# Kernel tuning notes

Hardware: AMD Instinct MI355X
Metric: run time of the kernel (lower is better)

## Reference

```python
import jax, jax.numpy as jnp
import numpy as np

EPS = 1e-6
H = 12  # num_heads


def _rms(x, w):
    return x / jnp.sqrt(jnp.mean(x * x, axis=-1, keepdims=True) + EPS) * w


def _rot_half(x):
    x1, x2 = jnp.split(x, 2, axis=-1)
    return jnp.concatenate([-x2, x1], axis=-1)


def _rope(t, cos, sin):
    # t: [B,H,N,hd]; cos/sin: [N,hd] broadcast
    return t * cos + _rot_half(t) * sin


def setup_inputs() -> dict:
    key = jax.random.key(0)
    B, N, D, Nc = 1, 2048, 768, 16
    hd = D // H
    mh = 4 * D
    ks = jax.random.split(key, 16)
    s = 0.02
    g = lambda k, shape, sc=1.0: jax.random.normal(k, shape, dtype=jnp.float32) * sc
    # real RoPE tables (half-duplicated layout to match rotate_half)
    inv = 1.0 / (10000.0 ** (np.arange(hd // 2, dtype=np.float64) / (hd // 2)))
    ang = np.arange(N, dtype=np.float64)[:, None] * inv[None, :]
    cos = jnp.asarray(np.concatenate([np.cos(ang), np.cos(ang)], -1), dtype=jnp.float32)
    sin = jnp.asarray(np.concatenate([np.sin(ang), np.sin(ang)], -1), dtype=jnp.float32)
    return {
        'x': g(ks[0], (B, N, D)),
        'c': g(ks[1], (B, D)),
        'cond': g(ks[2], (B, Nc, D)),
        'rope_cos': cos,
        'rope_sin': sin,
        'norm1_w': jnp.ones((D,), jnp.float32),
        'norm2_w': jnp.ones((D,), jnp.float32),
        'norm3_w': jnp.ones((D,), jnp.float32),
        'cond_norm_w': jnp.ones((D,), jnp.float32),
        'sa_qkv_w': g(ks[3], (3 * D, D), s),
        'sa_proj_w': g(ks[4], (D, D), s),
        'sa_proj_b': jnp.zeros((D,), jnp.float32),
        'sa_qn_w': jnp.ones((hd,), jnp.float32),
        'sa_kn_w': jnp.ones((hd,), jnp.float32),
        'ca_q_w': g(ks[5], (D, D), s),
        'ca_k_w': g(ks[6], (D, D), s),
        'ca_v_w': g(ks[7], (D, D), s),
        'ca_proj_w': g(ks[8], (D, D), s),
        'ca_proj_b': jnp.zeros((D,), jnp.float32),
        'ca_qn_w': jnp.ones((hd,), jnp.float32),
        'ca_kn_w': jnp.ones((hd,), jnp.float32),
        'mlp_w1': g(ks[9], (mh, D), s),
        'mlp_w2': g(ks[10], (D, mh), s),
        'mlp_w3': g(ks[11], (mh, D), s),
        'ada_w': g(ks[12], (9 * D, D), s),
        'ada_b': jnp.zeros((9 * D,), jnp.float32),
    }


def reference(x, c, cond, rope_cos, rope_sin, norm1_w, norm2_w, norm3_w, cond_norm_w,
              sa_qkv_w, sa_proj_w, sa_proj_b, sa_qn_w, sa_kn_w,
              ca_q_w, ca_k_w, ca_v_w, ca_proj_w, ca_proj_b, ca_qn_w, ca_kn_w,
              mlp_w1, mlp_w2, mlp_w3, ada_w, ada_b):
    B, N, D = x.shape
    hd = D // H
    scale = hd ** -0.5

    # adaLN modulation: SiLU(c) -> Linear -> 9 chunks of [B, D]
    mod = jax.nn.silu(c) @ ada_w.T + ada_b
    (sh_msa, sc_msa, g_msa, sh_ca, sc_ca, g_ca,
     sh_mlp, sc_mlp, g_mlp) = jnp.split(mod, 9, axis=1)

    def modulate(h, sh, sc):
        return h * (1.0 + sc[:, None, :]) + sh[:, None, :]

    # ---- self-attention with QK-norm + RoPE ----
    h = modulate(_rms(x, norm1_w), sh_msa, sc_msa)
    qkv = (h @ sa_qkv_w.T).reshape(B, N, 3, H, hd).transpose(2, 0, 3, 1, 4)  # [3,B,H,N,hd]
    q, k, v = qkv[0], qkv[1], qkv[2]
    q = _rope(_rms(q, sa_qn_w), rope_cos, rope_sin)
    k = _rope(_rms(k, sa_kn_w), rope_cos, rope_sin)
    attn = jax.nn.softmax(jnp.einsum('bhid,bhjd->bhij', q, k) * scale, axis=-1)
    o = jnp.einsum('bhij,bhjd->bhid', attn, v).transpose(0, 2, 1, 3).reshape(B, N, D)
    x = x + g_msa[:, None, :] * (o @ sa_proj_w.T + sa_proj_b)

    # ---- cross-attention (RoPE on q only) ----
    h = modulate(_rms(x, norm2_w), sh_ca, sc_ca)
    cn = _rms(cond, cond_norm_w)
    Nc = cond.shape[1]
    q = (h @ ca_q_w.T).reshape(B, N, H, hd).transpose(0, 2, 1, 3)
    k = (cn @ ca_k_w.T).reshape(B, Nc, H, hd).transpose(0, 2, 1, 3)
    v = (cn @ ca_v_w.T).reshape(B, Nc, H, hd).transpose(0, 2, 1, 3)
    q = _rope(_rms(q, ca_qn_w), rope_cos, rope_sin)
    k = _rms(k, ca_kn_w)
    attn = jax.nn.softmax(jnp.einsum('bhid,bhjd->bhij', q, k) * scale, axis=-1)
    o = jnp.einsum('bhij,bhjd->bhid', attn, v).transpose(0, 2, 1, 3).reshape(B, N, D)
    x = x + g_ca[:, None, :] * (o @ ca_proj_w.T + ca_proj_b)

    # ---- SwiGLU MLP ----
    h = modulate(_rms(x, norm3_w), sh_mlp, sc_mlp)
    x = x + g_mlp[:, None, :] * ((jax.nn.silu(h @ mlp_w1.T) * (h @ mlp_w3.T)) @ mlp_w2.T)
    return x
```

## Files before the change

### kernel.cpp

```cpp
#include <hip/hip_runtime.h>

typedef unsigned short u16;
typedef unsigned int u32;
typedef __attribute__((ext_vector_type(8))) short s16x8;
typedef __attribute__((ext_vector_type(4))) float f32x4;
typedef __attribute__((ext_vector_type(4))) int i32x4;

static __device__ __forceinline__ float bf2f(u16 u) {
    return __uint_as_float(((u32)u) << 16);
}
static __device__ __forceinline__ u16 f2bf(float f) {
    u32 x = __float_as_uint(f);
    return (u16)((x + 0x7fffu + ((x >> 16) & 1u)) >> 16);
}
static __device__ __forceinline__ i32x4 pack8(float4 a, float4 b) {
    u32 p0 = (u32)f2bf(a.x) | ((u32)f2bf(a.y) << 16);
    u32 p1 = (u32)f2bf(a.z) | ((u32)f2bf(a.w) << 16);
    u32 p2 = (u32)f2bf(b.x) | ((u32)f2bf(b.y) << 16);
    u32 p3 = (u32)f2bf(b.z) | ((u32)f2bf(b.w) << 16);
    return (i32x4){(int)p0, (int)p1, (int)p2, (int)p3};
}
static __device__ __forceinline__ float wave_sum(float v) {
#pragma unroll
    for (int off = 32; off > 0; off >>= 1) v += __shfl_xor(v, off);
    return v;
}
static __device__ __forceinline__ void gload16(const void* g, void* l) {
    __builtin_amdgcn_global_load_lds((const __attribute__((address_space(1))) void*)g,
                                     (__attribute__((address_space(3))) void*)l, 16, 0, 0);
}

__global__ __launch_bounds__(256) void cvt_bf16(const float* __restrict__ src,
                                                u16* __restrict__ dst, int n8) {
    int i = blockIdx.x * 256 + threadIdx.x;
    if (i >= n8) return;
    float4 a = *(const float4*)(src + (size_t)i * 8);
    float4 b = *(const float4*)(src + (size_t)i * 8 + 4);
    *(i32x4*)(dst + (size_t)i * 8) = pack8(a, b);
}

__global__ __launch_bounds__(256) void ada_gemm(const float* __restrict__ c,
                                                const float* __restrict__ adaw,
                                                const float* __restrict__ adab,
                                                float* __restrict__ mod) {
    int wid = blockIdx.x * 4 + (threadIdx.x >> 6);
    int lane = threadIdx.x & 63;
    float sum = 0.f;
#pragma unroll
    for (int i = 0; i < 12; ++i) {
        float cv = c[i * 64 + lane];
        cv = cv / (1.f + __expf(-cv));
        sum += cv * adaw[(size_t)wid * 768 + i * 64 + lane];
    }
    sum = wave_sum(sum);
    if (lane == 0) mod[wid] = sum + adab[wid];
}

__global__ __launch_bounds__(256) void rms_mod(const float* __restrict__ x,
                                               const float* __restrict__ w,
                                               const float* __restrict__ mod, int chunk,
                                               u16* __restrict__ out) {
    const int row = blockIdx.x;
    const int tid = threadIdx.x;
    const float* xr = x + (size_t)row * 768;
    float v0 = xr[tid], v1 = xr[256 + tid], v2 = xr[512 + tid];
    float ss = wave_sum(v0 * v0 + v1 * v1 + v2 * v2);
    __shared__ float red[4];
    if ((tid & 63) == 0) red[tid >> 6] = ss;
    __syncthreads();
    float rn = rsqrtf((red[0] + red[1] + red[2] + red[3]) * (1.f / 768.f) + 1e-6f);
    const float* sh = mod + chunk * 768;
    const float* sc = sh + 768;
    u16* orow = out + (size_t)row * 768;
    orow[tid]       = f2bf(v0 * rn * w[tid]       * (1.f + sc[tid])       + sh[tid]);
    orow[256 + tid] = f2bf(v1 * rn * w[256 + tid] * (1.f + sc[256 + tid]) + sh[256 + tid]);
    orow[512 + tid] = f2bf(v2 * rn * w[512 + tid] * (1.f + sc[512 + tid]) + sh[512 + tid]);
}

__global__ __launch_bounds__(256) void rms_plain(const float* __restrict__ x,
                                                 const float* __restrict__ w,
                                                 float* __restrict__ out) {
    const int row = blockIdx.x;
    const int tid = threadIdx.x;
    const float* xr = x + (size_t)row * 768;
    float v0 = xr[tid], v1 = xr[256 + tid], v2 = xr[512 + tid];
    float ss = wave_sum(v0 * v0 + v1 * v1 + v2 * v2);
    __shared__ float red[4];
    if ((tid & 63) == 0) red[tid >> 6] = ss;
    __syncthreads();
    float rn = rsqrtf((red[0] + red[1] + red[2] + red[3]) * (1.f / 768.f) + 1e-6f);
    float* orow = out + (size_t)row * 768;
    orow[tid]       = v0 * rn * w[tid];
    orow[256 + tid] = v1 * rn * w[256 + tid];
    orow[512 + tid] = v2 * rn * w[512 + tid];
}

template <int EPI, int BN>
__global__ __launch_bounds__(256) void gemm_bt4(const u16* __restrict__ A,
                                                const u16* __restrict__ Wb,
                                                int M, int N, int K,
                                                float* outf, u16* outb,
                                                const float* resid,
                                                const float* __restrict__ gate,
                                                const float* __restrict__ bias,
                                                int C, int R, int nxc) {
    constexpr int NB = BN / 32;
    __shared__ __align__(16) u16 As[2][128 * 32];
    __shared__ __align__(16) u16 Bs[2][BN * 32];
    const int tid = threadIdx.x;
    const int lane = tid & 63;
    const int w = tid >> 6;
    const int wr = w >> 1, wc = w & 1;
    const int sub = blockIdx.x;
    const int xcd = sub & 7, idx = sub >> 3;
    const int cx = xcd % nxc, cy = xcd / nxc;
    const int col0 = (cx * C + idx % C) * BN;
    const int row0 = (cy * R + idx / C) << 7;

    const int r0u = tid >> 2, s0u = (tid & 3) ^ (r0u & 3);
    const int r1u = (tid + 256) >> 2, s1u = (tid & 3) ^ (r1u & 3);
    const u16* a0 = A + (size_t)(row0 + r0u) * K + s0u * 8;
    const u16* a1 = A + (size_t)(row0 + r1u) * K + s1u * 8;
    const u16* b0 = Wb + (size_t)(col0 + r0u) * K + s0u * 8;
    const u16* b1 = Wb + (size_t)(col0 + r1u) * K + s1u * 8;

    f32x4 acc[4][NB];
#pragma unroll
    for (int m = 0; m < 4; ++m)
#pragma unroll
        for (int n = 0; n < NB; ++n) acc[m][n] = (f32x4){0.f, 0.f, 0.f, 0.f};

    const int nt = K >> 5;
    int cur = 0;
#define G4_STAGE(buf, k0)                                   \
    {                                                       \
        char* ad = (char*)As[buf] + w * 1024;               \
        char* bd = (char*)Bs[buf] + w * 1024;               \
        gload16(a0 + (k0), ad);                             \
        gload16(a1 + (k0), ad + 4096);                      \
        gload16(b0 + (k0), bd);                             \
        if constexpr (BN == 128) gload16(b1 + (k0), bd + 4096); \
    }
    G4_STAGE(0, 0)
    for (int t = 0; t < nt; ++t) {
        __syncthreads();
        if (t + 1 < nt) G4_STAGE(cur ^ 1, (t + 1) << 5)
        s16x8 af[4], bfv[NB];
#pragma unroll
        for (int m = 0; m < 4; ++m) {
            int ra = wr * 64 + m * 16 + (lane & 15);
            int u = (lane >> 4) ^ (ra & 3);
            af[m] = *(const s16x8*)((const char*)As[cur] + ra * 64 + u * 16);
        }
#pragma unroll
        for (int n = 0; n < NB; ++n) {
            int cb = wc * (BN / 2) + n * 16 + (lane & 15);
            int u = (lane >> 4) ^ (cb & 3);
            bfv[n] = *(const s16x8*)((const char*)Bs[cur] + cb * 64 + u * 16);
        }
#pragma unroll
        for (int m = 0; m < 4; ++m)
#pragma unroll
            for (int n = 0; n < NB; ++n)
                acc[m][n] = __builtin_amdgcn_mfma_f32_16x16x32_bf16(af[m], bfv[n], acc[m][n], 0, 0, 0);
        cur ^= 1;
    }
#undef G4_STAGE
#pragma unroll
    for (int m = 0; m < 4; ++m) {
#pragma unroll
        for (int n = 0; n < NB; ++n) {
#pragma unroll
            for (int i = 0; i < 4; ++i) {
                int r = row0 + wr * 64 + m * 16 + (lane >> 4) * 4 + i;
                int cc = col0 + wc * (BN / 2) + n * 16 + (lane & 15);
                size_t idx2 = (size_t)r * N + cc;
                float v = acc[m][n][i];
                if constexpr (EPI == 0) {
                    outf[idx2] = v;
                } else if constexpr (EPI == 1) {
                    outb[idx2] = f2bf(v);
                } else if constexpr (EPI == 2) {
                    float b = bias ? bias[cc] : 0.f;
                    outf[idx2] = resid[idx2] + gate[cc] * (v + b);
                }
            }
        }
    }
}

__global__ __launch_bounds__(256) void gemm_sk2(const u16* __restrict__ A,
                                                const u16* __restrict__ Wb,
                                                int M, int N, int K,
                                                u16* __restrict__ p0,
                                                u16* __restrict__ p1,
                                                int C, int R, int nxc,
                                                int nsub, int kslice) {
    __shared__ __align__(16) u16 As[2][128 * 32];
    __shared__ __align__(16) u16 Bs[2][64 * 32];
    const int tid = threadIdx.x;
    const int lane = tid & 63;
    const int w = tid >> 6;
    const int wr = w >> 1, wc = w & 1;
    const int sub = blockIdx.x % nsub;
    const int z = blockIdx.x / nsub;
    const int xcd = sub & 7, idx = sub >> 3;
    const int cx = xcd % nxc, cy = xcd / nxc;
    const int col0 = (cx * C + idx % C) << 6;
    const int row0 = (cy * R + idx / C) << 7;
    const int kbase = z * kslice;

    const int r0u = tid >> 2, s0u = (tid & 3) ^ (r0u & 3);
    const int r1u = (tid + 256) >> 2, s1u = (tid & 3) ^ (r1u & 3);
    const u16* a0 = A + (size_t)(row0 + r0u) * K + kbase + s0u * 8;
    const u16* a1 = A + (size_t)(row0 + r1u) * K + kbase + s1u * 8;
    const u16* b0 = Wb + (size_t)(col0 + r0u) * K + kbase + s0u * 8;

    f32x4 acc[4][2];
#pragma unroll
    for (int m = 0; m < 4; ++m)
#pragma unroll
        for (int n = 0; n < 2; ++n) acc[m][n] = (f32x4){0.f, 0.f, 0.f, 0.f};

    const int nt = kslice >> 5;
    int cur = 0;
#define SK_STAGE(buf, k0)                                   \
    {                                                       \
        char* ad = (char*)As[buf] + w * 1024;               \
        char* bd = (char*)Bs[buf] + w * 1024;               \
        gload16(a0 + (k0), ad);                             \
        gload16(a1 + (k0), ad + 4096);                      \
        gload16(b0 + (k0), bd);                             \
    }
    SK_STAGE(0, 0)
    for (int t = 0; t < nt; ++t) {
        __syncthreads();
        if (t + 1 < nt) SK_STAGE(cur ^ 1, (t + 1) << 5)
        s16x8 af[4], bfv[2];
#pragma unroll
        for (int m = 0; m < 4; ++m) {
            int ra = wr * 64 + m * 16 + (lane & 15);
            int u = (lane >> 4) ^ (ra & 3);
            af[m] = *(const s16x8*)((const char*)As[cur] + ra * 64 + u * 16);
        }
#pragma unroll
        for (int n = 0; n < 2; ++n) {
            int cb = wc * 32 + n * 16 + (lane & 15);
            int u = (lane >> 4) ^ (cb & 3);
            bfv[n] = *(const s16x8*)((const char*)Bs[cur] + cb * 64 + u * 16);
        }
#pragma unroll
        for (int m = 0; m < 4; ++m)
#pragma unroll
            for (int n = 0; n < 2; ++n)
                acc[m][n] = __builtin_amdgcn_mfma_f32_16x16x32_bf16(af[m], bfv[n], acc[m][n], 0, 0, 0);
        cur ^= 1;
    }
#undef SK_STAGE
    u16* po = z ? p1 : p0;
#pragma unroll
    for (int m = 0; m < 4; ++m)
#pragma unroll
        for (int n = 0; n < 2; ++n)
#pragma unroll
            for (int i = 0; i < 4; ++i) {
                int r = row0 + wr * 64 + m * 16 + (lane >> 4) * 4 + i;
                int cc = col0 + wc * 32 + n * 16 + (lane & 15);
                po[(size_t)r * N + cc] = f2bf(acc[m][n][i]);
            }
}

template <int MODE>
__global__ __launch_bounds__(256) void comb(const u16* __restrict__ pa,
                                            const u16* __restrict__ pb,
                                            const float* __restrict__ resid,
                                            const float* __restrict__ gate,
                                            const float* __restrict__ bias,
                                            float* __restrict__ outf) {
    int base = (blockIdx.x * 256 + threadIdx.x) * 8;
    int col = base % 768;
    s16x8 a = *(const s16x8*)(pa + base);
    s16x8 b = *(const s16x8*)(pb + base);
    float o[8];
#pragma unroll
    for (int e = 0; e < 8; ++e) {
        float s = bf2f((u16)a[e]) + bf2f((u16)b[e]);
        if constexpr (MODE == 0) {
            o[e] = s;
        } else {
            float bb = bias ? bias[col + e] : 0.f;
            o[e] = resid[base + e] + gate[col + e] * (s + bb);
        }
    }
    *(float4*)(outf + base) = (float4){o[0], o[1], o[2], o[3]};
    *(float4*)(outf + base + 4) = (float4){o[4], o[5], o[6], o[7]};
}

__global__ __launch_bounds__(256) void gemm_w13(const u16* __restrict__ A,
                                                const u16* __restrict__ W1,
                                                const float* __restrict__ W3,
                                                int M, int N, int K,
                                                u16* __restrict__ outb,
                                                int C, int R, int nxc) {
    __shared__ __align__(16) u16 As[2][128 * 32];
    __shared__ __align__(16) u16 B1s[2][64 * 32];
    __shared__ __align__(16) float B3s[2][64 * 32];
    const int tid = threadIdx.x;
    const int lane = tid & 63;
    const int w = tid >> 6;
    const int wr = w >> 1, wc = w & 1;
    const int sub = blockIdx.x;
    const int xcd = sub & 7, idx = sub >> 3;
    const int cx = xcd % nxc, cy = xcd / nxc;
    const int col0 = (cx * C + idx % C) << 6;
    const int row0 = (cy * R + idx / C) << 7;

    const int r0u = tid >> 2, s0u = (tid & 3) ^ (r0u & 3);
    const int r1u = (tid + 256) >> 2, s1u = (tid & 3) ^ (r1u & 3);
    const u16* a0 = A + (size_t)(row0 + r0u) * K + s0u * 8;
    const u16* a1 = A + (size_t)(row0 + r1u) * K + s1u * 8;
    const u16* b1p = W1 + (size_t)(col0 + r0u) * K + s0u * 8;
    const int v0r = tid >> 3, v0g = (tid & 7) >> 1, v0h = tid & 1;
    const int v0s = v0g ^ (v0r & 3);
    const int v1u = tid + 256;
    const int v1r = v1u >> 3, v1g = (v1u & 7) >> 1, v1h = v1u & 1;
    const int v1s = v1g ^ (v1r & 3);
    const float* b3p0 = W3 + (size_t)(col0 + v0r) * K + v0s * 8 + v0h * 4;
    const float* b3p1 = W3 + (size_t)(col0 + v1r) * K + v1s * 8 + v1h * 4;

    f32x4 acc1[4][2], acc3[4][2];
#pragma unroll
    for (int m = 0; m < 4; ++m)
#pragma unroll
        for (int n = 0; n < 2; ++n) {
            acc1[m][n] = (f32x4){0.f, 0.f, 0.f, 0.f};
            acc3[m][n] = (f32x4){0.f, 0.f, 0.f, 0.f};
        }

    const int nt = K >> 5;
    int cur = 0;
#define W13_STAGE(buf, k0)                                  \
    {                                                       \
        char* ad = (char*)As[buf] + w * 1024;               \
        char* bd1 = (char*)B1s[buf] + w * 1024;             \
        char* bd3 = (char*)B3s[buf] + w * 1024;             \
        gload16(a0 + (k0), ad);                             \
        gload16(a1 + (k0), ad + 4096);                      \
        gload16(b1p + (k0), bd1);                           \
        gload16(b3p0 + (k0), bd3);                          \
        gload16(b3p1 + (k0), bd3 + 4096);                   \
    }
    W13_STAGE(0, 0)
    for (int t = 0; t < nt; ++t) {
        __syncthreads();
        if (t + 1 < nt) W13_STAGE(cur ^ 1, (t + 1) << 5)
        s16x8 af[4], b1v[2], b3v[2];
#pragma unroll
        for (int m = 0; m < 4; ++m) {
            int ra = wr * 64 + m * 16 + (lane & 15);
            int u = (lane >> 4) ^ (ra & 3);
            af[m] = *(const s16x8*)((const char*)As[cur] + ra * 64 + u * 16);
        }
#pragma unroll
        for (int n = 0; n < 2; ++n) {
            int cb = wc * 32 + n * 16 + (lane & 15);
            int u = (lane >> 4) ^ (cb & 3);
            b1v[n] = *(const s16x8*)((const char*)B1s[cur] + cb * 64 + u * 16);
            const char* vb = (const char*)B3s[cur] + cb * 128 + u * 32;
            float4 lo = *(const float4*)vb;
            float4 hi = *(const float4*)(vb + 16);
            i32x4 p = pack8(lo, hi);
            b3v[n] = *(s16x8*)&p;
        }
#pragma unroll
        for (int m = 0; m < 4; ++m)
#pragma unroll
            for (int n = 0; n < 2; ++n) {
                acc1[m][n] = __builtin_amdgcn_mfma_f32_16x16x32_bf16(af[m], b1v[n], acc1[m][n], 0, 0, 0);
                acc3[m][n] = __builtin_amdgcn_mfma_f32_16x16x32_bf16(af[m], b3v[n], acc3[m][n], 0, 0, 0);
            }
        cur ^= 1;
    }
#undef W13_STAGE
#pragma unroll
    for (int m = 0; m < 4; ++m)
#pragma unroll
        for (int n = 0; n < 2; ++n)
#pragma unroll
            for (int i = 0; i < 4; ++i) {
                int r = row0 + wr * 64 + m * 16 + (lane >> 4) * 4 + i;
                int cc = col0 + wc * 32 + n * 16 + (lane & 15);
                float v1 = acc1[m][n][i];
                float g = v1 / (1.f + __expf(-v1));
                outb[(size_t)r * N + cc] = f2bf(g * acc3[m][n][i]);
            }
}

__global__ __launch_bounds__(256) void saqk_rmsrope(u16* __restrict__ qkv,
                                                    const float* __restrict__ qnw,
                                                    const float* __restrict__ knw,
                                                    const float* __restrict__ cosT,
                                                    const float* __restrict__ sinT) {
    int wid = blockIdx.x * 4 + (threadIdx.x >> 6);
    int lane = threadIdx.x & 63;
    int n = wid / 24;
    int rem = wid % 24;
    int which = rem / 12;
    int h = rem % 12;
    u16* p = qkv + (size_t)n * 2304 + which * 768 + h * 64 + lane;
    float v = bf2f(*p);
    float ss = wave_sum(v * v);
    const float* wv = which ? knw : qnw;
    float vn = v * rsqrtf(ss * (1.f / 64.f) + 1e-6f) * wv[lane];
    float part = __shfl_xor(vn, 32);
    float rot = (lane < 32) ? -part : part;
    *p = f2bf(vn * cosT[n * 64 + lane] + rot * sinT[n * 64 + lane]);
}

__global__ __launch_bounds__(256) void v_transpose(const u16* __restrict__ qkv,
                                                   u16* __restrict__ vT) {
    const int kt = blockIdx.x, h = blockIdx.y;
    const int tid = threadIdx.x;
    __shared__ __align__(16) u16 tt[64][72];
    {
        int key = tid >> 2, qq = tid & 3;
        const u16* src = qkv + (size_t)(kt * 64 + key) * 2304 + 1536 + h * 64 + qq * 16;
        *(i32x4*)&tt[key][qq * 16]     = *(const i32x4*)src;
        *(i32x4*)&tt[key][qq * 16 + 8] = *(const i32x4*)(src + 8);
    }
    __syncthreads();
    {
        int d = tid >> 2, kq = tid & 3;
        s16x8 o0, o1;
#pragma unroll
        for (int e = 0; e < 8; ++e) o0[e] = (short)tt[kq * 16 + e][d];
#pragma unroll
        for (int e = 0; e < 8; ++e) o1[e] = (short)tt[kq * 16 + 8 + e][d];
        u16* dst = vT + (size_t)h * 131072 + (size_t)d * 2048 + kt * 64 + kq * 16;
        *(s16x8*)dst = o0;
        *(s16x8*)(dst + 8) = o1;
    }
}

__global__ __launch_bounds__(256) void sa_attn_mfma(const u16* __restrict__ qkv,
                                                    const u16* __restrict__ vT,
                                                    u16* __restrict__ po0,
                                                    u16* __restrict__ po1,
                                                    float* __restrict__ pl) {
    const int h = blockIdx.y;
    const int r0 = blockIdx.x * 64;
    const int z = blockIdx.z;
    const int tid = threadIdx.x;
    const int lane = tid & 63;
    const int w = tid >> 6;
    __shared__ __align__(16) u16 Ks[2][64 * 64];
    __shared__ __align__(16) u16 Vs[2][64 * 64];
    __shared__ __align__(16) u16 Ps[4][16 * 64];

    s16x8 qf[2];
    {
        const u16* qrow = qkv + (size_t)(r0 + w * 16 + (lane & 15)) * 2304 + h * 64 + ((lane >> 4) * 8);
        qf[0] = *(const s16x8*)qrow;
        qf[1] = *(const s16x8*)(qrow + 32);
    }
    f32x4 oacc[4];
#pragma unroll
    for (int n = 0; n < 4; ++n) oacc[n] = (f32x4){0.f, 0.f, 0.f, 0.f};
    float lp[4] = {0.f, 0.f, 0.f, 0.f};

    const u16* ksrc[2];
    const u16* vsrc[2];
#pragma unroll
    for (int j = 0; j < 2; ++j) {
        int u = (w * 2 + j) * 64 + lane;
        int row = u >> 3, seg = (u & 7) ^ (row & 7);
        ksrc[j] = qkv + (size_t)(z * 1024 + row) * 2304 + 768 + h * 64 + seg * 8;
        vsrc[j] = vT + (size_t)h * 131072 + (size_t)row * 2048 + z * 1024 + seg * 8;
    }

#define SA_STAGE(buf, t_)                                          \
    {                                                              \
        char* kd = (char*)Ks[buf] + w * 2048;                      \
        char* vd = (char*)Vs[buf] + w * 2048;                      \
        gload16(ksrc[0] + (size_t)(t_) * 147456, kd);              \
        gload16(ksrc[1] + (size_t)(t_) * 147456, kd + 1024);       \
        gload16(vsrc[0] + (t_) * 64, vd);                          \
        gload16(vsrc[1] + (t_) * 64, vd + 1024);                   \
    }

    SA_STAGE(0, 0)
    int cur = 0;
    for (int t = 0; t < 16; ++t) {
        __syncthreads();
        if (t + 1 < 16) SA_STAGE(cur ^ 1, t + 1)

        f32x4 sacc[4];
#pragma unroll
        for (int n = 0; n < 4; ++n) sacc[n] = (f32x4){0.f, 0.f, 0.f, 0.f};
#pragma unroll
        for (int kk = 0; kk < 2; ++kk) {
#pragma unroll
            for (int n = 0; n < 4; ++n) {
                int key = n * 16 + (lane & 15);
                int d = kk * 32 + (lane >> 4) * 8;
                int boff = key * 128 + ((d * 2) ^ ((key & 7) << 4));
                s16x8 kf = *(const s16x8*)((const char*)Ks[cur] + boff);
                sacc[n] = __builtin_amdgcn_mfma_f32_16x16x32_bf16(qf[kk], kf, sacc[n], 0, 0, 0);
            }
        }
#pragma unroll
        for (int n = 0; n < 4; ++n) {
#pragma unroll
            for (int i = 0; i < 4; ++i) {
                float p = __expf(fmaf(sacc[n][i], 0.125f, -8.0f));
                lp[i] += p;
                int row = (lane >> 4) * 4 + i;
                int key = n * 16 + (lane & 15);
                int boff = row * 128 + ((key * 2) ^ ((row & 7) << 4));
                *(u16*)((char*)Ps[w] + boff) = f2bf(p);
            }
        }
#pragma unroll
        for (int kk = 0; kk < 2; ++kk) {
            int koff = kk * 32 + (lane >> 4) * 8;
            int prow = lane & 15;
            int pboff = prow * 128 + ((koff * 2) ^ ((prow & 7) << 4));
            s16x8 pf = *(const s16x8*)((const char*)Ps[w] + pboff);
#pragma unroll
            for (int n = 0; n < 4; ++n) {
                int d = n * 16 + (lane & 15);
                int vboff = d * 128 + ((koff * 2) ^ ((d & 7) << 4));
                s16x8 vf = *(const s16x8*)((const char*)Vs[cur] + vboff);
                oacc[n] = __builtin_amdgcn_mfma_f32_16x16x32_bf16(pf, vf, oacc[n], 0, 0, 0);
            }
        }
        cur ^= 1;
    }
#undef SA_STAGE
#pragma unroll
    for (int off = 1; off < 16; off <<= 1) {
#pragma unroll
        for (int i = 0; i < 4; ++i) lp[i] += __shfl_xor(lp[i], off);
    }
    u16* po = z ? po1 : po0;
#pragma unroll
    for (int n = 0; n < 4; ++n) {
#pragma unroll
        for (int i = 0; i < 4; ++i) {
            int r = r0 + w * 16 + (lane >> 4) * 4 + i;
            int d = n * 16 + (lane & 15);
            po[(size_t)r * 768 + h * 64 + d] = f2bf(oacc[n][i]);
        }
    }
    if ((lane & 15) == 0) {
#pragma unroll
        for (int i = 0; i < 4; ++i) {
            int r = r0 + w * 16 + (lane >> 4) * 4 + i;
            pl[z * 24576 + h * 2048 + r] = lp[i];
        }
    }
}

__global__ __launch_bounds__(256) void sa_combine(const u16* __restrict__ pa,
                                                  const u16* __restrict__ pb,
                                                  const float* __restrict__ pl,
                                                  u16* __restrict__ obuf) {
    int idx = blockIdx.x * 256 + threadIdx.x;
    int base = idx * 8;
    int row = base / 768;
    int col = base % 768;
    int h = col >> 6;
    float inv = 1.f / (pl[h * 2048 + row] + pl[24576 + h * 2048 + row]);
    s16x8 a = *(const s16x8*)(pa + base);
    s16x8 b = *(const s16x8*)(pb + base);
    s16x8 o;
#pragma unroll
    for (int e = 0; e < 8; ++e)
        o[e] = (short)f2bf((bf2f((u16)a[e]) + bf2f((u16)b[e])) * inv);
    *(s16x8*)(obuf + base) = o;
}

__global__ __launch_bounds__(256) void ca_attn(const float* __restrict__ qb,
                                               const float* __restrict__ kca,
                                               const float* __restrict__ vca,
                                               u16* __restrict__ obuf) {
    int wid = blockIdx.x * 4 + (threadIdx.x >> 6);
    int lane = threadIdx.x & 63;
    int n = wid / 12, h = wid % 12;
    float qd = qb[(size_t)n * 768 + h * 64 + lane] * 0.125f;
    float s[16];
#pragma unroll
    for (int j = 0; j < 16; ++j) {
        float part = qd * kca[(size_t)j * 768 + h * 64 + lane];
        s[j] = wave_sum(part);
    }
    float mm = s[0];
#pragma unroll
    for (int j = 1; j < 16; ++j) mm = fmaxf(mm, s[j]);
    float l = 0.f;
#pragma unroll
    for (int j = 0; j < 16; ++j) { s[j] = __expf(s[j] - mm); l += s[j]; }
    float od = 0.f;
#pragma unroll
    for (int j = 0; j < 16; ++j) od += s[j] * vca[(size_t)j * 768 + h * 64 + lane];
    obuf[(size_t)n * 768 + h * 64 + lane] = f2bf(od / l);
}

__global__ __launch_bounds__(256) void caq_rmsrope(float* __restrict__ qb,
                                                   const float* __restrict__ qnw,
                                                   const float* __restrict__ cosT,
                                                   const float* __restrict__ sinT) {
    int wid = blockIdx.x * 4 + (threadIdx.x >> 6);
    int lane = threadIdx.x & 63;
    int n = wid / 12, h = wid % 12;
    float* p = qb + (size_t)n * 768 + h * 64 + lane;
    float v = *p;
    float ss = wave_sum(v * v);
    float vn = v * rsqrtf(ss * (1.f / 64.f) + 1e-6f) * qnw[lane];
    float part = __shfl_xor(vn, 32);
    float rot = (lane < 32) ? -part : part;
    *p = vn * cosT[n * 64 + lane] + rot * sinT[n * 64 + lane];
}

__global__ __launch_bounds__(256) void cak_rms(float* __restrict__ kca,
                                               const float* __restrict__ knw) {
    int wid = blockIdx.x * 4 + (threadIdx.x >> 6);
    int lane = threadIdx.x & 63;
    int n = wid / 12, h = wid % 12;
    float* p = kca + (size_t)n * 768 + h * 64 + lane;
    float v = *p;
    float ss = wave_sum(v * v);
    *p = v * rsqrtf(ss * (1.f / 64.f) + 1e-6f) * knw[lane];
}

__global__ __launch_bounds__(256) void small_gemm_nt(const float* __restrict__ cn,
                                                     const float* __restrict__ cakw,
                                                     const float* __restrict__ cavw,
                                                     float* __restrict__ kca,
                                                     float* __restrict__ vca) {
    int wid = blockIdx.x * 4 + (threadIdx.x >> 6);
    int lane = threadIdx.x & 63;
    int which = wid / 12288;
    int rem = wid % 12288;
    int rrow = rem / 768;
    int ocol = rem % 768;
    const float* Wm = which ? cavw : cakw;
    float sum = 0.f;
#pragma unroll
    for (int i = 0; i < 12; ++i)
        sum += cn[(size_t)rrow * 768 + i * 64 + lane] * Wm[(size_t)ocol * 768 + i * 64 + lane];
    sum = wave_sum(sum);
    if (lane == 0) (which ? vca : kca)[(size_t)rrow * 768 + ocol] = sum;
}

extern "C" void kernel_launch(void* const* d_in, const int* in_sizes, int n_in,
                              void* d_out, int out_size, void* d_ws, size_t ws_size,
                              hipStream_t stream) {
    const float* x     = (const float*)d_in[0];
    const float* c     = (const float*)d_in[1];
    const float* cond  = (const float*)d_in[2];
    const float* cosT  = (const float*)d_in[3];
    const float* sinT  = (const float*)d_in[4];
    const float* n1w   = (const float*)d_in[5];
    const float* n2w   = (const float*)d_in[6];
    const float* n3w   = (const float*)d_in[7];
    const float* cnw   = (const float*)d_in[8];
    const float* saqkvw  = (const float*)d_in[9];
    const float* saprojw = (const float*)d_in[10];
    const float* saprojb = (const float*)d_in[11];
    const float* saqnw   = (const float*)d_in[12];
    const float* saknw   = (const float*)d_in[13];
    const float* caqw    = (const float*)d_in[14];
    const float* cakw    = (const float*)d_in[15];
    const float* cavw    = (const float*)d_in[16];
    const float* caprojw = (const float*)d_in[17];
    const float* caprojb = (const float*)d_in[18];
    const float* caqnw   = (const float*)d_in[19];
    const float* caknw   = (const float*)d_in[20];
    const float* w1      = (const float*)d_in[21];
    const float* w2      = (const float*)d_in[22];
    const float* w3      = (const float*)d_in[23];
    const float* adaw    = (const float*)d_in[24];
    const float* adab    = (const float*)d_in[25];
    float* out = (float*)d_out;
    char* ws = (char*)d_ws;

    float* mod  = (float*)ws;
    u16* hbuf   = (u16*)(ws + 32768);
    u16* obuf   = (u16*)(ws + 3178496);
    char* R1    = ws + 6324224;
    u16* qkvb   = (u16*)R1;
    u16* vTb    = (u16*)(R1 + 9437184);
    float* qbuf = (float*)R1;
    u16* gbuf   = (u16*)R1;
    float* cn   = (float*)(ws + 18907136);
    float* kca  = (float*)(ws + 18956288);
    float* vca  = (float*)(ws + 19005440);
    u16* wbuf   = (u16*)(ws + 19054592);
    u16* po0    = hbuf;
    u16* po1    = wbuf;
    float* plb  = (float*)(ws + 22200320);
    u16* skA0 = (u16*)R1;
    u16* skA1 = (u16*)(R1 + 3145728);
    u16* skQ0 = (u16*)(R1 + 6291456);
    u16* skQ1 = (u16*)(R1 + 9437184);
    u16* skW0 = hbuf;
    u16* skW1 = obuf;

    ada_gemm<<<1728, 256, 0, stream>>>(c, adaw, adab, mod);

    rms_mod<<<2048, 256, 0, stream>>>(x, n1w, mod, 0, hbuf);
    cvt_bf16<<<864, 256, 0, stream>>>(saqkvw, wbuf, 221184);
    gemm_bt4<1, 64><<<576, 256, 0, stream>>>(hbuf, wbuf, 2048, 2304, 768,
                                             nullptr, qkvb, nullptr, nullptr, nullptr,
                                             9, 8, 4);
    saqk_rmsrope<<<12288, 256, 0, stream>>>(qkvb, saqnw, saknw, cosT, sinT);
    v_transpose<<<dim3(32, 12), 256, 0, stream>>>(qkvb, vTb);
    sa_attn_mfma<<<dim3(32, 12, 2), 256, 0, stream>>>(qkvb, vTb, po0, po1, plb);
    sa_combine<<<768, 256, 0, stream>>>(po0, po1, plb, obuf);
    cvt_bf16<<<288, 256, 0, stream>>>(saprojw, wbuf, 73728);
    gemm_sk2<<<384, 256, 0, stream>>>(obuf, wbuf, 2048, 768, 768,
                                      skA0, skA1, 6, 4, 2, 192, 384);
    comb<2><<<768, 256, 0, stream>>>(skA0, skA1, x, mod + 2 * 768, saprojb, out);

    rms_mod<<<2048, 256, 0, stream>>>(out, n2w, mod, 3, hbuf);
    cvt_bf16<<<288, 256, 0, stream>>>(caqw, wbuf, 73728);
    gemm_sk2<<<384, 256, 0, stream>>>(hbuf, wbuf, 2048, 768, 768,
                                      skQ0, skQ1, 6, 4, 2, 192, 384);
    comb<0><<<768, 256, 0, stream>>>(skQ0, skQ1, nullptr, nullptr, nullptr, qbuf);
    rms_plain<<<16, 256, 0, stream>>>(cond, cnw, cn);
    small_gemm_nt<<<6144, 256, 0, stream>>>(cn, cakw, cavw, kca, vca);
    cak_rms<<<48, 256, 0, stream>>>(kca, caknw);
    caq_rmsrope<<<6144, 256, 0, stream>>>(qbuf, caqnw, cosT, sinT);
    ca_attn<<<6144, 256, 0, stream>>>(qbuf, kca, vca, obuf);
    cvt_bf16<<<288, 256, 0, stream>>>(caprojw, wbuf, 73728);
    gemm_sk2<<<384, 256, 0, stream>>>(obuf, wbuf, 2048, 768, 768,
                                      skA0, skA1, 6, 4, 2, 192, 384);
    comb<2><<<768, 256, 0, stream>>>(skA0, skA1, out, mod + 5 * 768, caprojb, out);

    rms_mod<<<2048, 256, 0, stream>>>(out, n3w, mod, 6, hbuf);
    cvt_bf16<<<1152, 256, 0, stream>>>(w1, wbuf, 294912);
    gemm_w13<<<768, 256, 0, stream>>>(hbuf, wbuf, w3, 2048, 3072, 768,
                                      gbuf, 12, 8, 4);
    cvt_bf16<<<1152, 256, 0, stream>>>(w2, wbuf, 294912);
    gemm_sk2<<<384, 256, 0, stream>>>(gbuf, wbuf, 2048, 768, 3072,
                                      skW0, skW1, 6, 4, 2, 192, 1536);
    comb<2><<<768, 256, 0, stream>>>(skW0, skW1, out, mod + 8 * 768, nullptr, out);
}
```

Baseline: 252.1 us.

## Use 4-way split-K for GEMMs and attention, fuse combine with RMSNorm, pre-convert W3

Split-K for the 768-output GEMMs and the KV split in self-attention go from 2-way to 4-way, with partials written into one strided workspace and reduced by new 4-input combine kernels. This doubles the number of blocks to fill more CUs. The residual-gated combine is fused with the following RMSNorm+modulate into a per-row kernel, which removes the separate rms_mod launches and a re-read of the output. W3 is now converted to bf16 upfront, so gemm_w13 loads bf16 tiles instead of fp32 and no longer packs them in the inner loop. The cost is more partial-sum memory traffic, an extra conversion kernel, and reduced-precision bf16 partials being summed four ways.

Result: faster. 241.8 us (-4.1%).

```diff
diff --git a/kernel.cpp b/kernel.cpp
--- a/kernel.cpp
+++ b/kernel.cpp
@@ -5,6 +5,8 @@
 typedef __attribute__((ext_vector_type(8))) short s16x8;
 typedef __attribute__((ext_vector_type(4))) float f32x4;
 typedef __attribute__((ext_vector_type(4))) int i32x4;
+
+#define PS 1572864
 
 static __device__ __forceinline__ float bf2f(u16 u) {
     return __uint_as_float(((u32)u) << 16);
@@ -189,11 +191,10 @@
     }
 }
 
-__global__ __launch_bounds__(256) void gemm_sk2(const u16* __restrict__ A,
+__global__ __launch_bounds__(256) void gemm_sk4(const u16* __restrict__ A,
                                                 const u16* __restrict__ Wb,
                                                 int M, int N, int K,
-                                                u16* __restrict__ p0,
-                                                u16* __restrict__ p1,
+                                                u16* __restrict__ pz,
                                                 int C, int R, int nxc,
                                                 int nsub, int kslice) {
     __shared__ __align__(16) u16 As[2][128 * 32];
@@ -257,7 +258,7 @@
         cur ^= 1;
     }
 #undef SK_STAGE
-    u16* po = z ? p1 : p0;
+    u16* po = pz + (size_t)z * PS;
 #pragma unroll
     for (int m = 0; m < 4; ++m)
 #pragma unroll
@@ -271,20 +272,22 @@
 }
 
 template <int MODE>
-__global__ __launch_bounds__(256) void comb(const u16* __restrict__ pa,
-                                            const u16* __restrict__ pb,
-                                            const float* __restrict__ resid,
-                                            const float* __restrict__ gate,
-                                            const float* __restrict__ bias,
-                                            float* __restrict__ outf) {
+__global__ __launch_bounds__(256) void comb4(const u16* __restrict__ pz,
+                                             const float* __restrict__ resid,
+                                             const float* __restrict__ gate,
+                                             const float* __restrict__ bias,
+                                             float* __restrict__ outf) {
     int base = (blockIdx.x * 256 + threadIdx.x) * 8;
     int col = base % 768;
-    s16x8 a = *(const s16x8*)(pa + base);
-    s16x8 b = *(const s16x8*)(pb + base);
+    s16x8 p0 = *(const s16x8*)(pz + base);
+    s16x8 p1 = *(const s16x8*)(pz + PS + base);
+    s16x8 p2 = *(const s16x8*)(pz + 2 * PS + base);
+    s16x8 p3 = *(const s16x8*)(pz + 3 * PS + base);
     float o[8];
 #pragma unroll
     for (int e = 0; e < 8; ++e) {
-        float s = bf2f((u16)a[e]) + bf2f((u16)b[e]);
+        float s = (bf2f((u16)p0[e]) + bf2f((u16)p1[e])) +
+                  (bf2f((u16)p2[e]) + bf2f((u16)p3[e]));
         if constexpr (MODE == 0) {
             o[e] = s;
         } else {
@@ -296,15 +299,54 @@
     *(float4*)(outf + base + 4) = (float4){o[4], o[5], o[6], o[7]};
 }
 
+__global__ __launch_bounds__(256) void comb_rms(const u16* __restrict__ pz,
+                                                const float* __restrict__ resid,
+                                                const float* __restrict__ gate,
+                                                const float* __restrict__ bias,
+                                                const float* __restrict__ mod, int chunk,
+                                                const float* __restrict__ w,
+                                                float* __restrict__ outf,
+                                                u16* __restrict__ outb) {
+    const int row = blockIdx.x;
+    const int tid = threadIdx.x;
+    float val[3];
+    float ss = 0.f;
+#pragma unroll
+    for (int j = 0; j < 3; ++j) {
+        int col = tid + j * 256;
+        size_t ix = (size_t)row * 768 + col;
+        float s = (bf2f(pz[ix]) + bf2f(pz[PS + ix])) +
+                  (bf2f(pz[2 * PS + ix]) + bf2f(pz[3 * PS + ix]));
+        float bb = bias ? bias[col] : 0.f;
+        float v = resid[ix] + gate[col] * (s + bb);
+        val[j] = v;
+        ss += v * v;
+        outf[ix] = v;
+    }
+    ss = wave_sum(ss);
+    __shared__ float red[4];
+    if ((tid & 63) == 0) red[tid >> 6] = ss;
+    __syncthreads();
+    float rn = rsqrtf((red[0] + red[1] + red[2] + red[3]) * (1.f / 768.f) + 1e-6f);
+    const float* sh = mod + chunk * 768;
+    const float* sc = sh + 768;
+#pragma unroll
+    for (int j = 0; j < 3; ++j) {
+        int col = tid + j * 256;
+        size_t ix = (size_t)row * 768 + col;
+        outb[ix] = f2bf(val[j] * rn * w[col] * (1.f + sc[col]) + sh[col]);
+    }
+}
+
 __global__ __launch_bounds__(256) void gemm_w13(const u16* __restrict__ A,
                                                 const u16* __restrict__ W1,
-                                                const float* __restrict__ W3,
+                                                const u16* __restrict__ W3,
                                                 int M, int N, int K,
                                                 u16* __restrict__ outb,
                                                 int C, int R, int nxc) {
     __shared__ __align__(16) u16 As[2][128 * 32];
     __shared__ __align__(16) u16 B1s[2][64 * 32];
-    __shared__ __align__(16) float B3s[2][64 * 32];
+    __shared__ __align__(16) u16 B3s[2][64 * 32];
     const int tid = threadIdx.x;
     const int lane = tid & 63;
     const int w = tid >> 6;
@@ -320,13 +362,7 @@
     const u16* a0 = A + (size_t)(row0 + r0u) * K + s0u * 8;
     const u16* a1 = A + (size_t)(row0 + r1u) * K + s1u * 8;
     const u16* b1p = W1 + (size_t)(col0 + r0u) * K + s0u * 8;
-    const int v0r = tid >> 3, v0g = (tid & 7) >> 1, v0h = tid & 1;
-    const int v0s = v0g ^ (v0r & 3);
-    const int v1u = tid + 256;
-    const int v1r = v1u >> 3, v1g = (v1u & 7) >> 1, v1h = v1u & 1;
-    const int v1s = v1g ^ (v1r & 3);
-    const float* b3p0 = W3 + (size_t)(col0 + v0r) * K + v0s * 8 + v0h * 4;
-    const float* b3p1 = W3 + (size_t)(col0 + v1r) * K + v1s * 8 + v1h * 4;
+    const u16* b3p = W3 + (size_t)(col0 + r0u) * K + s0u * 8;
 
     f32x4 acc1[4][2], acc3[4][2];
 #pragma unroll
@@ -347,8 +383,7 @@
         gload16(a0 + (k0), ad);                             \
         gload16(a1 + (k0), ad + 4096);                      \
         gload16(b1p + (k0), bd1);                           \
-        gload16(b3p0 + (k0), bd3);                          \
-        gload16(b3p1 + (k0), bd3 + 4096);                   \
+        gload16(b3p + (k0), bd3);                           \
     }
     W13_STAGE(0, 0)
     for (int t = 0; t < nt; ++t) {
@@ -366,11 +401,7 @@
             int cb = wc * 32 + n * 16 + (lane & 15);
             int u = (lane >> 4) ^ (cb & 3);
             b1v[n] = *(const s16x8*)((const char*)B1s[cur] + cb * 64 + u * 16);
-            const char* vb = (const char*)B3s[cur] + cb * 128 + u * 32;
-            float4 lo = *(const float4*)vb;
-            float4 hi = *(const float4*)(vb + 16);
-            i32x4 p = pack8(lo, hi);
-            b3v[n] = *(s16x8*)&p;
+            b3v[n] = *(const s16x8*)((const char*)B3s[cur] + cb * 64 + u * 16);
         }
 #pragma unroll
         for (int m = 0; m < 4; ++m)
@@ -444,8 +475,7 @@
 
 __global__ __launch_bounds__(256) void sa_attn_mfma(const u16* __restrict__ qkv,
                                                     const u16* __restrict__ vT,
-                                                    u16* __restrict__ po0,
-                                                    u16* __restrict__ po1,
+                                                    u16* __restrict__ at,
                                                     float* __restrict__ pl) {
     const int h = blockIdx.y;
     const int r0 = blockIdx.x * 64;
@@ -474,8 +504,8 @@
     for (int j = 0; j < 2; ++j) {
         int u = (w * 2 + j) * 64 + lane;
         int row = u >> 3, seg = (u & 7) ^ (row & 7);
-        ksrc[j] = qkv + (size_t)(z * 1024 + row) * 2304 + 768 + h * 64 + seg * 8;
-        vsrc[j] = vT + (size_t)h * 131072 + (size_t)row * 2048 + z * 1024 + seg * 8;
+        ksrc[j] = qkv + (size_t)(z * 512 + row) * 2304 + 768 + h * 64 + seg * 8;
+        vsrc[j] = vT + (size_t)h * 131072 + (size_t)row * 2048 + z * 512 + seg * 8;
     }
 
 #define SA_STAGE(buf, t_)                                          \
@@ -490,9 +520,9 @@
 
     SA_STAGE(0, 0)
     int cur = 0;
-    for (int t = 0; t < 16; ++t) {
+    for (int t = 0; t < 8; ++t) {
         __syncthreads();
-        if (t + 1 < 16) SA_STAGE(cur ^ 1, t + 1)
+        if (t + 1 < 8) SA_STAGE(cur ^ 1, t + 1)
 
         f32x4 sacc[4];
 #pragma unroll
@@ -542,7 +572,7 @@
 #pragma unroll
         for (int i = 0; i < 4; ++i) lp[i] += __shfl_xor(lp[i], off);
     }
-    u16* po = z ? po1 : po0;
+    u16* po = at + (size_t)z * PS;
 #pragma unroll
     for (int n = 0; n < 4; ++n) {
 #pragma unroll
@@ -561,22 +591,28 @@
     }
 }
 
-__global__ __launch_bounds__(256) void sa_combine(const u16* __restrict__ pa,
-                                                  const u16* __restrict__ pb,
-                                                  const float* __restrict__ pl,
-                                                  u16* __restrict__ obuf) {
+__global__ __launch_bounds__(256) void sa_combine4(const u16* __restrict__ at,
+                                                   const float* __restrict__ pl,
+                                                   u16* __restrict__ obuf) {
     int idx = blockIdx.x * 256 + threadIdx.x;
     int base = idx * 8;
     int row = base / 768;
     int col = base % 768;
     int h = col >> 6;
-    float inv = 1.f / (pl[h * 2048 + row] + pl[24576 + h * 2048 + row]);
-    s16x8 a = *(const s16x8*)(pa + base);
-    s16x8 b = *(const s16x8*)(pb + base);
+    float l = (pl[h * 2048 + row] + pl[24576 + h * 2048 + row]) +
+              (pl[49152 + h * 2048 + row] + pl[73728 + h * 2048 + row]);
+    float inv = 1.f / l;
+    s16x8 a = *(const s16x8*)(at + base);
+    s16x8 b = *(const s16x8*)(at + PS + base);
+    s16x8 cc = *(const s16x8*)(at + 2 * PS + base);
+    s16x8 d = *(const s16x8*)(at + 3 * PS + base);
     s16x8 o;
 #pragma unroll
-    for (int e = 0; e < 8; ++e)
-        o[e] = (short)f2bf((bf2f((u16)a[e]) + bf2f((u16)b[e])) * inv);
+    for (int e = 0; e < 8; ++e) {
+        float s = (bf2f((u16)a[e]) + bf2f((u16)b[e])) +
+                  (bf2f((u16)cc[e]) + bf2f((u16)d[e]));
+        o[e] = (short)f2bf(s * inv);
+    }
     *(s16x8*)(obuf + base) = o;
 }
 
@@ -697,15 +733,10 @@
     float* kca  = (float*)(ws + 18956288);
     float* vca  = (float*)(ws + 19005440);
     u16* wbuf   = (u16*)(ws + 19054592);
-    u16* po0    = hbuf;
-    u16* po1    = wbuf;
-    float* plb  = (float*)(ws + 22200320);
-    u16* skA0 = (u16*)R1;
-    u16* skA1 = (u16*)(R1 + 3145728);
-    u16* skQ0 = (u16*)(R1 + 6291456);
-    u16* skQ1 = (u16*)(R1 + 9437184);
-    u16* skW0 = hbuf;
-    u16* skW1 = obuf;
+    u16* AT     = (u16*)(ws + 25165824);
+    float* PL4  = (float*)(ws + 37748736);
+    u16* WB3    = (u16*)(ws + 38141952);
+    u16* SKP    = (u16*)(ws + 42860544);
 
     ada_gemm<<<1728, 256, 0, stream>>>(c, adaw, adab, mod);
 
@@ -716,34 +747,35 @@
                                              9, 8, 4);
     saqk_rmsrope<<<12288, 256, 0, stream>>>(qkvb, saqnw, saknw, cosT, sinT);
     v_transpose<<<dim3(32, 12), 256, 0, stream>>>(qkvb, vTb);
-    sa_attn_mfma<<<dim3(32, 12, 2), 256, 0, stream>>>(qkvb, vTb, po0, po1, plb);
-    sa_combine<<<768, 256, 0, stream>>>(po0, po1, plb, obuf);
+    sa_attn_mfma<<<dim3(32, 12, 4), 256, 0, stream>>>(qkvb, vTb, AT, PL4);
+    sa_combine4<<<768, 256, 0, stream>>>(AT, PL4, obuf);
     cvt_bf16<<<288, 256, 0, stream>>>(saprojw, wbuf, 73728);
-    gemm_sk2<<<384, 256, 0, stream>>>(obuf, wbuf, 2048, 768, 768,
-                                      skA0, skA1, 6, 4, 2, 192, 384);
-    comb<2><<<768, 256, 0, stream>>>(skA0, skA1, x, mod + 2 * 768, saprojb, out);
-
-    rms_mod<<<2048, 256, 0, stream>>>(out, n2w, mod, 3, hbuf);
+    gemm_sk4<<<768, 256, 0, stream>>>(obuf, wbuf, 2048, 768, 768,
+                                      SKP, 6, 4, 2, 192, 192);
+    comb_rms<<<2048, 256, 0, stream>>>(SKP, x, mod + 2 * 768, saprojb,
+                                       mod, 3, n2w, out, hbuf);
+
     cvt_bf16<<<288, 256, 0, stream>>>(caqw, wbuf, 73728);
-    gemm_sk2<<<384, 256, 0, stream>>>(hbuf, wbuf, 2048, 768, 768,
-                                      skQ0, skQ1, 6, 4, 2, 192, 384);
-    comb<0><<<768, 256, 0, stream>>>(skQ0, skQ1, nullptr, nullptr, nullptr, qbuf);
+    gemm_sk4<<<768, 256, 0, stream>>>(hbuf, wbuf, 2048, 768, 768,
+                                      SKP, 6, 4, 2, 192, 192);
+    comb4<0><<<768, 256, 0, stream>>>(SKP, nullptr, nullptr, nullptr, qbuf);
     rms_plain<<<16, 256, 0, stream>>>(cond, cnw, cn);
     small_gemm_nt<<<6144, 256, 0, stream>>>(cn, cakw, cavw, kca, vca);
     cak_rms<<<48, 256, 0, stream>>>(kca, caknw);
     caq_rmsrope<<<6144, 256, 0, stream>>>(qbuf, caqnw, cosT, sinT);
     ca_attn<<<6144, 256, 0, stream>>>(qbuf, kca, vca, obuf);
     cvt_bf16<<<288, 256, 0, stream>>>(caprojw, wbuf, 73728);
-    gemm_sk2<<<384, 256, 0, stream>>>(obuf, wbuf, 2048, 768, 768,
-                                      skA0, skA1, 6, 4, 2, 192, 384);
-    comb<2><<<768, 256, 0, stream>>>(skA0, skA1, out, mod + 5 * 768, caprojb, out);
-
-    rms_mod<<<2048, 256, 0, stream>>>(out, n3w, mod, 6, hbuf);
+    gemm_sk4<<<768, 256, 0, stream>>>(obuf, wbuf, 2048, 768, 768,
+                                      SKP, 6, 4, 2, 192, 192);
+    comb_rms<<<2048, 256, 0, stream>>>(SKP, out, mod + 5 * 768, caprojb,
+                                       mod, 6, n3w, out, hbuf);
+
     cvt_bf16<<<1152, 256, 0, stream>>>(w1, wbuf, 294912);
-    gemm_w13<<<768, 256, 0, stream>>>(hbuf, wbuf, w3, 2048, 3072, 768,
+    cvt_bf16<<<1152, 256, 0, stream>>>(w3, WB3, 294912);
+    gemm_w13<<<768, 256, 0, stream>>>(hbuf, wbuf, WB3, 2048, 3072, 768,
                                       gbuf, 12, 8, 4);
     cvt_bf16<<<1152, 256, 0, stream>>>(w2, wbuf, 294912);
-    gemm_sk2<<<384, 256, 0, stream>>>(gbuf, wbuf, 2048, 768, 3072,
-                                      skW0, skW1, 6, 4, 2, 192, 1536);
-    comb<2><<<768, 256, 0, stream>>>(skW0, skW1, out, mod + 8 * 768, nullptr, out);
-}
+    gemm_sk4<<<768, 256, 0, stream>>>(gbuf, wbuf, 2048, 768, 3072,
+                                      SKP, 6, 4, 2, 192, 768);
+    comb4<2><<<768, 256, 0, stream>>>(SKP, out, mod + 8 * 768, nullptr, out);
+}
```
